# Kernel tuning notes

Measured on AMD Instinct MI355X. Metric: run time of the kernel, lower is better.

## Reference

```python
import jax, jax.numpy as jnp
import numpy as np


def setup_inputs() -> dict:
    key = jax.random.key(0)
    k1, k2, k3 = jax.random.split(key, 3)
    B, T1, T2, D = 16, 1024, 1024, 256
    x = jax.random.normal(k1, (B, T1, D), dtype=jnp.float32)
    y = jax.random.normal(k2, (B, T2, D), dtype=jnp.float32)
    WS = jax.random.normal(k3, (3 * D,), dtype=jnp.float32) * 0.05
    return {"x": x, "y": y, "WS": WS}


def reference(x, y, WS):
    # BiDAF trilinear similarity. Original computes
    #   S[b,i,j] = sum_k concat([x_i, 1, x_i])_k * concat([1, y_j, y_j])_k * WS_k
    # which decomposes exactly into:
    #   S = x @ w1 (broadcast over j) + y @ w2 (broadcast over i) + (x * w3) @ y^T
    D = x.shape[-1]
    w1, w2, w3 = WS[:D], WS[D:2 * D], WS[2 * D:]
    term_x = jnp.einsum('bid,d->bi', x, w1)            # [B, T1]
    term_y = jnp.einsum('bjd,d->bj', y, w2)            # [B, T2]
    term_xy = jnp.einsum('bid,bjd->bij', x * w3, y)    # [B, T1, T2]
    return term_xy + term_x[:, :, None] + term_y[:, None, :]
```

## Files before the change

kernel.cpp:

```cpp
#include <hip/hip_runtime.h>

#define DK 256
#define TT 1024
#define NB 16

typedef __attribute__((ext_vector_type(8))) short bf16x8;
typedef __attribute__((ext_vector_type(4))) float f32x4;

__device__ __forceinline__ unsigned int cvt_pk_bf16(float lo, float hi) {
    unsigned int r;
    asm("v_cvt_pk_bf16_f32 %0, %1, %2" : "=v"(r) : "v"(lo), "v"(hi));
    return r;
}

union BF8 { uint4 u; bf16x8 v; };


__global__ __launch_bounds__(256) void prep_kernel(
    const float* __restrict__ x, const float* __restrict__ y,
    const float* __restrict__ WS,
    unsigned short* __restrict__ xb, unsigned short* __restrict__ yb,
    float* __restrict__ tx, float* __restrict__ ty)
{
    const int lane = threadIdx.x & 63;
    const int gw   = blockIdx.x * 4 + (threadIdx.x >> 6);
    const int r    = gw & 16383;
    const bool isx = gw < 16384;

    const float* src = (isx ? x : y) + (size_t)r * DK + lane * 4;
    const float4 v  = *(const float4*)src;
    const float4 wd = *(const float4*)(WS + (isx ? 0 : DK) + lane * 4);

    float dot = v.x * wd.x + v.y * wd.y + v.z * wd.z + v.w * wd.w;
    dot += __shfl_xor(dot, 1);
    dot += __shfl_xor(dot, 2);
    dot += __shfl_xor(dot, 4);
    dot += __shfl_xor(dot, 8);
    dot += __shfl_xor(dot, 16);
    dot += __shfl_xor(dot, 32);

    float4 s = v;
    if (!isx) {
        const float4 w3 = *(const float4*)(WS + 2 * DK + lane * 4);
        s.x = v.x * w3.x; s.y = v.y * w3.y; s.z = v.z * w3.z; s.w = v.w * w3.w;
    }
    uint2 o;
    o.x = cvt_pk_bf16(s.x, s.y);
    o.y = cvt_pk_bf16(s.z, s.w);

    if (isx) {
        *(uint2*)(xb + (size_t)r * DK + lane * 4) = o;
    } else {
        const int c = lane >> 1;
        const int h = lane & 1;
        *(uint2*)(yb + (size_t)r * DK + ((c ^ (r & 7)) * 8 + h * 4)) = o;
    }
    if (lane == 0) (isx ? tx : ty)[r] = dot;
}

__global__ __launch_bounds__(512, 4) void gemm_kernel(
    const unsigned short* __restrict__ xb, const unsigned short* __restrict__ yb,
    const float* __restrict__ tx, const float* __restrict__ ty,
    float* __restrict__ out)
{
    __shared__ unsigned short Bs[128 * DK];
    __shared__ float txs[256];
    __shared__ float tys[128];

    const int tid  = threadIdx.x;
    const int lane = tid & 63;
    const int w    = tid >> 6;

    const int id = blockIdx.x;
    const int b  = id & 15;
    const int is = (id >> 4) & 3;
    const int jt = id >> 6;

    const int mfr  = lane & 15;
    const int quad = lane >> 4;
    const int i0   = is * 256 + w * 32;
    const unsigned short* gA = xb + ((size_t)b * TT + i0) * DK;

    uint4 a[4][2];
    #pragma unroll
    for (int ks = 0; ks < 4; ++ks)
        #pragma unroll
        for (int it = 0; it < 2; ++it)
            a[ks][it] = *(const uint4*)(gA + (size_t)(it * 16 + mfr) * DK
                                        + ks * 32 + quad * 8);

    {
        const unsigned short* gY = yb + ((size_t)b * TT + jt * 128) * DK;
        #pragma unroll
        for (int it = 0; it < 8; ++it) {
            const int g = it * 512 + w * 64 + lane;
            const unsigned short* gp = gY + (size_t)g * 8;
            unsigned short* lp = Bs + (size_t)(it * 512 + w * 64) * 8;
            __builtin_amdgcn_global_load_lds(
                (const __attribute__((address_space(1))) void*)gp,
                (__attribute__((address_space(3))) void*)lp, 16, 0, 0);
        }
        if (tid < 64)
            *(float4*)&txs[tid * 4] =
                *(const float4*)(tx + b * TT + is * 256 + tid * 4);
        else if (tid < 96)
            *(float4*)&tys[(tid - 64) * 4] =
                *(const float4*)(ty + b * TT + jt * 128 + (tid - 64) * 4);
    }
    __syncthreads();

    f32x4 acc[2][8];
    #pragma unroll
    for (int it = 0; it < 2; ++it)
        #pragma unroll
        for (int n = 0; n < 8; ++n)
            acc[it][n] = (f32x4){0.f, 0.f, 0.f, 0.f};

    #pragma unroll
    for (int ks = 0; ks < 8; ++ks) {
        bf16x8 av[2];
        #pragma unroll
        for (int it = 0; it < 2; ++it) {
            BF8 cv;
            cv.u = a[ks & 3][it];
            av[it] = cv.v;
        }
        if (ks < 4) {
            #pragma unroll
            for (int it = 0; it < 2; ++it)
                a[ks & 3][it] = *(const uint4*)(gA
                    + (size_t)(it * 16 + mfr) * DK + (ks + 4) * 32 + quad * 8);
        }
        #pragma unroll
        for (int n = 0; n < 8; ++n) {
            const int j    = n * 16 + mfr;
            const int slot = (ks * 4 + quad) ^ (j & 7);
            const bf16x8 bv = *(const bf16x8*)(Bs + j * DK + slot * 8);
            #pragma unroll
            for (int it = 0; it < 2; ++it)
                acc[it][n] = __builtin_amdgcn_mfma_f32_16x16x32_bf16(
                    av[it], bv, acc[it][n], 0, 0, 0);
        }
    }

    float tyv[8];
    #pragma unroll
    for (int n = 0; n < 8; ++n)
        tyv[n] = tys[n * 16 + mfr];

    float* outB = out + ((size_t)b << 20) + (size_t)i0 * TT + jt * 128;
    #pragma unroll
    for (int it = 0; it < 2; ++it) {
        #pragma unroll
        for (int r = 0; r < 4; ++r) {
            const int row  = it * 16 + quad * 4 + r;
            const float trow = txs[w * 32 + row];
            #pragma unroll
            for (int n = 0; n < 8; ++n)
                outB[(size_t)row * TT + n * 16 + mfr] =
                    acc[it][n][r] + trow + tyv[n];
        }
    }
}

__global__ __launch_bounds__(512, 4) void fused_kernel(
    const float* __restrict__ x, const float* __restrict__ y,
    const float* __restrict__ WS, float* __restrict__ out)
{
    __shared__ unsigned short Bs[128 * DK];
    __shared__ float tys[128];

    const int tid  = threadIdx.x;
    const int lane = tid & 63;
    const int w    = tid >> 6;

    const int id = blockIdx.x;
    const int b  = id & 15;
    const int is = (id >> 4) & 3;
    const int jt = id >> 6;

    {
        const float* gY0 = y + ((size_t)b * TT + jt * 128) * DK;
        const int c = tid & 31;
        const float* w3p = WS + 2 * DK + c * 8;
        const float* w2p = WS + DK + c * 8;
        const float4 wa = *(const float4*)(w3p);
        const float4 wb = *(const float4*)(w3p + 4);
        const float4 va = *(const float4*)(w2p);
        const float4 vb = *(const float4*)(w2p + 4);
        #pragma unroll
        for (int it = 0; it < 8; ++it) {
            const int j = it * 16 + (tid >> 5);
            const float* gY = gY0 + (size_t)j * DK + c * 8;
            const float4 ya = *(const float4*)(gY);
            const float4 yb2 = *(const float4*)(gY + 4);
            float p = ya.x * va.x + ya.y * va.y + ya.z * va.z + ya.w * va.w
                    + yb2.x * vb.x + yb2.y * vb.y + yb2.z * vb.z + yb2.w * vb.w;
            uint4 o;
            o.x = cvt_pk_bf16(ya.x * wa.x, ya.y * wa.y);
            o.y = cvt_pk_bf16(ya.z * wa.z, ya.w * wa.w);
            o.z = cvt_pk_bf16(yb2.x * wb.x, yb2.y * wb.y);
            o.w = cvt_pk_bf16(yb2.z * wb.z, yb2.w * wb.w);
            const int slot = c ^ (j & 7);
            *(uint4*)(Bs + j * DK + slot * 8) = o;
            p += __shfl_xor(p, 1);
            p += __shfl_xor(p, 2);
            p += __shfl_xor(p, 4);
            p += __shfl_xor(p, 8);
            p += __shfl_xor(p, 16);
            if ((tid & 31) == 0) tys[j] = p;
        }
    }
    __syncthreads();

    const int mfr  = lane & 15;
    const int quad = lane >> 4;
    const int i0   = is * 256 + w * 32;
    const float* gA = x + ((size_t)b * TT + i0) * DK;

    f32x4 acc[2][8];
    #pragma unroll
    for (int it = 0; it < 2; ++it)
        #pragma unroll
        for (int n = 0; n < 8; ++n)
            acc[it][n] = (f32x4){0.f, 0.f, 0.f, 0.f};
    float txp[2] = {0.f, 0.f};

    #pragma unroll
    for (int ks = 0; ks < 8; ++ks) {
        const float* w1p = WS + ks * 32 + quad * 8;
        const float4 w1a = *(const float4*)(w1p);
        const float4 w1b = *(const float4*)(w1p + 4);
        bf16x8 av[2];
        #pragma unroll
        for (int it = 0; it < 2; ++it) {
            const float* rp = gA + (size_t)(it * 16 + mfr) * DK
                              + ks * 32 + quad * 8;
            const float4 xa = *(const float4*)rp;
            const float4 xb2 = *(const float4*)(rp + 4);
            txp[it] += xa.x * w1a.x + xa.y * w1a.y + xa.z * w1a.z + xa.w * w1a.w
                     + xb2.x * w1b.x + xb2.y * w1b.y + xb2.z * w1b.z + xb2.w * w1b.w;
            BF8 cv;
            cv.u.x = cvt_pk_bf16(xa.x, xa.y);
            cv.u.y = cvt_pk_bf16(xa.z, xa.w);
            cv.u.z = cvt_pk_bf16(xb2.x, xb2.y);
            cv.u.w = cvt_pk_bf16(xb2.z, xb2.w);
            av[it] = cv.v;
        }
        #pragma unroll
        for (int n = 0; n < 8; ++n) {
            const int j    = n * 16 + mfr;
            const int slot = (ks * 4 + quad) ^ (j & 7);
            const bf16x8 bv = *(const bf16x8*)(Bs + j * DK + slot * 8);
            #pragma unroll
            for (int it = 0; it < 2; ++it)
                acc[it][n] = __builtin_amdgcn_mfma_f32_16x16x32_bf16(
                    av[it], bv, acc[it][n], 0, 0, 0);
        }
    }

    #pragma unroll
    for (int it = 0; it < 2; ++it) {
        txp[it] += __shfl_xor(txp[it], 16);
        txp[it] += __shfl_xor(txp[it], 32);
    }

    float tyv[8];
    #pragma unroll
    for (int n = 0; n < 8; ++n)
        tyv[n] = tys[n * 16 + mfr];

    float* outB = out + ((size_t)b << 20) + (size_t)i0 * TT + jt * 128;
    #pragma unroll
    for (int it = 0; it < 2; ++it) {
        #pragma unroll
        for (int r = 0; r < 4; ++r) {
            const int row = it * 16 + quad * 4 + r;
            const float trow = __shfl(txp[it], (lane & 48) | (quad * 4 + r));
            #pragma unroll
            for (int n = 0; n < 8; ++n)
                outB[(size_t)row * TT + n * 16 + mfr] =
                    acc[it][n][r] + trow + tyv[n];
        }
    }
}

extern "C" void kernel_launch(void* const* d_in, const int* in_sizes, int n_in,
                              void* d_out, int out_size, void* d_ws, size_t ws_size,
                              hipStream_t stream)
{
    const float* x  = (const float*)d_in[0];
    const float* y  = (const float*)d_in[1];
    const float* WS = (const float*)d_in[2];
    float* out = (float*)d_out;

    const size_t XB_OFF = 0;
    const size_t YB_OFF = 8388608;
    const size_t TX_OFF = 16777216;
    const size_t TY_OFF = 16842752;
    const size_t NEED   = 16908288;

    if (ws_size >= NEED && d_ws != nullptr) {
        unsigned short* xb = (unsigned short*)((char*)d_ws + XB_OFF);
        unsigned short* yb = (unsigned short*)((char*)d_ws + YB_OFF);
        float* tx = (float*)((char*)d_ws + TX_OFF);
        float* ty = (float*)((char*)d_ws + TY_OFF);
        prep_kernel<<<dim3(8192), dim3(256), 0, stream>>>(x, y, WS, xb, yb, tx, ty);
        gemm_kernel<<<dim3(512), dim3(512), 0, stream>>>(xb, yb, tx, ty, out);
    } else {
        fused_kernel<<<dim3(512), dim3(512), 0, stream>>>(x, y, WS, out);
    }
}
```

Baseline: 107.5 us.

## Widen gemm block tile to 256 columns reusing A fragments across two B tiles

Each GEMM block now computes a 256-column output tile by loading two 128-row Y tiles into double-sized LDS and reusing the full A fragment held in registers for both halves. This halves the number of blocks (512 to 256) and halves redundant reads of the x operand. The cost is twice the LDS per block and more registers (all 8 k-slices of A kept live), with launch bounds lowered to 2 blocks per CU. With only 256 blocks on a 256-CU part, occupancy and latency hiding drop.

```diff
diff --git a/kernel.cpp b/kernel.cpp
--- a/kernel.cpp
+++ b/kernel.cpp
@@ -58,107 +58,103 @@
     if (lane == 0) (isx ? tx : ty)[r] = dot;
 }
 
-__global__ __launch_bounds__(512, 4) void gemm_kernel(
+__global__ __launch_bounds__(512, 2) void gemm_kernel(
     const unsigned short* __restrict__ xb, const unsigned short* __restrict__ yb,
     const float* __restrict__ tx, const float* __restrict__ ty,
     float* __restrict__ out)
 {
-    __shared__ unsigned short Bs[128 * DK];
+    __shared__ unsigned short Bs[2][128 * DK];
     __shared__ float txs[256];
-    __shared__ float tys[128];
+    __shared__ float tys[256];
 
     const int tid  = threadIdx.x;
     const int lane = tid & 63;
     const int w    = tid >> 6;
 
-    const int id = blockIdx.x;
-    const int b  = id & 15;
-    const int is = (id >> 4) & 3;
-    const int jt = id >> 6;
+    const int id  = blockIdx.x;
+    const int b   = id & 15;
+    const int is  = (id >> 4) & 3;
+    const int jtg = id >> 6;
 
     const int mfr  = lane & 15;
     const int quad = lane >> 4;
     const int i0   = is * 256 + w * 32;
     const unsigned short* gA = xb + ((size_t)b * TT + i0) * DK;
 
-    uint4 a[4][2];
-    #pragma unroll
-    for (int ks = 0; ks < 4; ++ks)
+    uint4 a[8][2];
+    #pragma unroll
+    for (int ks = 0; ks < 8; ++ks)
         #pragma unroll
         for (int it = 0; it < 2; ++it)
             a[ks][it] = *(const uint4*)(gA + (size_t)(it * 16 + mfr) * DK
                                         + ks * 32 + quad * 8);
 
-    {
-        const unsigned short* gY = yb + ((size_t)b * TT + jt * 128) * DK;
+    #pragma unroll
+    for (int h = 0; h < 2; ++h) {
+        const unsigned short* gY =
+            yb + ((size_t)b * TT + jtg * 256 + h * 128) * DK;
         #pragma unroll
         for (int it = 0; it < 8; ++it) {
             const int g = it * 512 + w * 64 + lane;
             const unsigned short* gp = gY + (size_t)g * 8;
-            unsigned short* lp = Bs + (size_t)(it * 512 + w * 64) * 8;
+            unsigned short* lp = &Bs[h][(size_t)(it * 512 + w * 64) * 8];
             __builtin_amdgcn_global_load_lds(
                 (const __attribute__((address_space(1))) void*)gp,
                 (__attribute__((address_space(3))) void*)lp, 16, 0, 0);
         }
-        if (tid < 64)
-            *(float4*)&txs[tid * 4] =
-                *(const float4*)(tx + b * TT + is * 256 + tid * 4);
-        else if (tid < 96)
-            *(float4*)&tys[(tid - 64) * 4] =
-                *(const float4*)(ty + b * TT + jt * 128 + (tid - 64) * 4);
-    }
+    }
+    if (tid < 64)
+        *(float4*)&txs[tid * 4] =
+            *(const float4*)(tx + b * TT + is * 256 + tid * 4);
+    else if (tid < 128)
+        *(float4*)&tys[(tid - 64) * 4] =
+            *(const float4*)(ty + b * TT + jtg * 256 + (tid - 64) * 4);
     __syncthreads();
 
-    f32x4 acc[2][8];
-    #pragma unroll
-    for (int it = 0; it < 2; ++it)
-        #pragma unroll
-        for (int n = 0; n < 8; ++n)
-            acc[it][n] = (f32x4){0.f, 0.f, 0.f, 0.f};
-
-    #pragma unroll
-    for (int ks = 0; ks < 8; ++ks) {
-        bf16x8 av[2];
+    float* outT = out + ((size_t)b << 20) + (size_t)i0 * TT + jtg * 256;
+
+    #pragma unroll
+    for (int h = 0; h < 2; ++h) {
+        f32x4 acc[2][8];
+        #pragma unroll
+        for (int it = 0; it < 2; ++it)
+            #pragma unroll
+            for (int n = 0; n < 8; ++n)
+                acc[it][n] = (f32x4){0.f, 0.f, 0.f, 0.f};
+
+        #pragma unroll
+        for (int ks = 0; ks < 8; ++ks) {
+            bf16x8 av[2];
+            #pragma unroll
+            for (int it = 0; it < 2; ++it) {
+                BF8 cv;
+                cv.u = a[ks][it];
+                av[it] = cv.v;
+            }
+            #pragma unroll
+            for (int n = 0; n < 8; ++n) {
+                const int j    = n * 16 + mfr;
+                const int slot = (ks * 4 + quad) ^ (j & 7);
+                const bf16x8 bv = *(const bf16x8*)(&Bs[h][j * DK + slot * 8]);
+                #pragma unroll
+                for (int it = 0; it < 2; ++it)
+                    acc[it][n] = __builtin_amdgcn_mfma_f32_16x16x32_bf16(
+                        av[it], bv, acc[it][n], 0, 0, 0);
+            }
+        }
+
+        float* outB = outT + h * 128;
         #pragma unroll
         for (int it = 0; it < 2; ++it) {
-            BF8 cv;
-            cv.u = a[ks & 3][it];
-            av[it] = cv.v;
-        }
-        if (ks < 4) {
-            #pragma unroll
-            for (int it = 0; it < 2; ++it)
-                a[ks & 3][it] = *(const uint4*)(gA
-                    + (size_t)(it * 16 + mfr) * DK + (ks + 4) * 32 + quad * 8);
-        }
-        #pragma unroll
-        for (int n = 0; n < 8; ++n) {
-            const int j    = n * 16 + mfr;
-            const int slot = (ks * 4 + quad) ^ (j & 7);
-            const bf16x8 bv = *(const bf16x8*)(Bs + j * DK + slot * 8);
-            #pragma unroll
-            for (int it = 0; it < 2; ++it)
-                acc[it][n] = __builtin_amdgcn_mfma_f32_16x16x32_bf16(
-                    av[it], bv, acc[it][n], 0, 0, 0);
-        }
-    }
-
-    float tyv[8];
-    #pragma unroll
-    for (int n = 0; n < 8; ++n)
-        tyv[n] = tys[n * 16 + mfr];
-
-    float* outB = out + ((size_t)b << 20) + (size_t)i0 * TT + jt * 128;
-    #pragma unroll
-    for (int it = 0; it < 2; ++it) {
-        #pragma unroll
-        for (int r = 0; r < 4; ++r) {
-            const int row  = it * 16 + quad * 4 + r;
-            const float trow = txs[w * 32 + row];
-            #pragma unroll
-            for (int n = 0; n < 8; ++n)
-                outB[(size_t)row * TT + n * 16 + mfr] =
-                    acc[it][n][r] + trow + tyv[n];
+            #pragma unroll
+            for (int r = 0; r < 4; ++r) {
+                const int row  = it * 16 + quad * 4 + r;
+                const float trow = txs[w * 32 + row];
+                #pragma unroll
+                for (int n = 0; n < 8; ++n)
+                    outB[(size_t)row * TT + n * 16 + mfr] =
+                        acc[it][n][r] + trow + tys[h * 128 + n * 16 + mfr];
+            }
         }
     }
 }
@@ -306,7 +302,7 @@
         float* tx = (float*)((char*)d_ws + TX_OFF);
         float* ty = (float*)((char*)d_ws + TY_OFF);
         prep_kernel<<<dim3(8192), dim3(256), 0, stream>>>(x, y, WS, xb, yb, tx, ty);
-        gemm_kernel<<<dim3(512), dim3(512), 0, stream>>>(xb, yb, tx, ty, out);
+        gemm_kernel<<<dim3(256), dim3(512), 0, stream>>>(xb, yb, tx, ty, out);
     } else {
         fused_kernel<<<dim3(512), dim3(512), 0, stream>>>(x, y, WS, out);
     }
```

After: 109.8 us. 1.02x slower.
